# Performance work log

Hardware: AMD Instinct MI355X
Metric: run time of the kernel (lower is better)

Reference implementation:

```python
import jax, jax.numpy as jnp
import numpy as np

B, S, H, D = 2, 2048, 16, 64

def setup_inputs() -> dict:
    key = jax.random.key(0)
    kq, kk, kv = jax.random.split(key, 3)
    query = jax.random.normal(kq, (B, S, H, D), dtype=jnp.float32)
    k_ = jax.random.normal(kk, (B, S, H, D), dtype=jnp.float32)
    v_ = jax.random.normal(kv, (B, S, H, D), dtype=jnp.float32)
    return {"query": query, "key": k_, "value": v_}

def reference(query, key, value):
    # AsyncLongContextAttention with world_size=1 degenerates to full
    # softmax attention over the global sequence (all2all / ring are
    # pure data movement). Defaults: causal=False, dropout_p=0.0,
    # softmax_scale = 1/sqrt(head_dim) (flash-attn convention).
    scale = 1.0 / jnp.sqrt(jnp.asarray(query.shape[-1], query.dtype))
    # scores: [B, H, Sq, Sk]
    scores = jnp.einsum("bqhd,bkhd->bhqk", query, key) * scale
    probs = jax.nn.softmax(scores, axis=-1)
    # out: [B, Sq, H, D]
    out = jnp.einsum("bhqk,bkhd->bqhd", probs, value)
    return out
```

## Files before the change

kernel.cpp:

```cpp
#include <hip/hip_runtime.h>
#include <math.h>

using half8  = __attribute__((ext_vector_type(8))) _Float16;
using half4  = __attribute__((ext_vector_type(4))) _Float16;
using fp16x2 = __attribute__((ext_vector_type(2))) __fp16;
using f32x4  = __attribute__((ext_vector_type(4))) float;

namespace {
constexpr int NB = 2, NS = 2048, NH = 16, ND = 64;
constexpr int QBLK = 128, KVBLK = 64;
constexpr int RS = NH * ND;
constexpr int NT = NS / KVBLK;
constexpr size_t TILEH = 4096;
constexpr size_t TILEB = TILEH * 2;
constexpr size_t SCR_HALFS = (size_t)NB * NH * NT * TILEH;

__device__ __forceinline__ int sidx(int row, int col) {
    return row * 64 + (col ^ (((row & 7) ^ ((row >> 3) & 7)) << 3));
}
__device__ __forceinline__ int kperm(int k) {
    return 16 * (2 * (k >> 5) + ((k >> 2) & 1)) + 4 * ((k >> 3) & 3) + (k & 3);
}
__device__ __forceinline__ float ex2(float x) {
#if __has_builtin(__builtin_amdgcn_exp2f)
    return __builtin_amdgcn_exp2f(x);
#else
    return exp2f(x);
#endif
}
__device__ __forceinline__ half8 pk8(const float4& a, const float4& b) {
    half8 r;
    fp16x2* h = (fp16x2*)&r;
    h[0] = __builtin_amdgcn_cvt_pkrtz(a.x, a.y);
    h[1] = __builtin_amdgcn_cvt_pkrtz(a.z, a.w);
    h[2] = __builtin_amdgcn_cvt_pkrtz(b.x, b.y);
    h[3] = __builtin_amdgcn_cvt_pkrtz(b.z, b.w);
    return r;
}
__device__ __forceinline__ half8 pk8s(const float4& a, const float4& b, float s) {
    half8 r;
    fp16x2* h = (fp16x2*)&r;
    h[0] = __builtin_amdgcn_cvt_pkrtz(a.x * s, a.y * s);
    h[1] = __builtin_amdgcn_cvt_pkrtz(a.z * s, a.w * s);
    h[2] = __builtin_amdgcn_cvt_pkrtz(b.x * s, b.y * s);
    h[3] = __builtin_amdgcn_cvt_pkrtz(b.z * s, b.w * s);
    return r;
}
__device__ __forceinline__ half8 pk8v(const float* v) {
    half8 r;
    fp16x2* h = (fp16x2*)&r;
    h[0] = __builtin_amdgcn_cvt_pkrtz(v[0], v[1]);
    h[1] = __builtin_amdgcn_cvt_pkrtz(v[2], v[3]);
    h[2] = __builtin_amdgcn_cvt_pkrtz(v[4], v[5]);
    h[3] = __builtin_amdgcn_cvt_pkrtz(v[6], v[7]);
    return r;
}
__device__ __forceinline__ half8 pkq(const f32x4& a, const f32x4& b) {
    half8 r;
    fp16x2* h = (fp16x2*)&r;
    h[0] = __builtin_amdgcn_cvt_pkrtz(a[0], a[1]);
    h[1] = __builtin_amdgcn_cvt_pkrtz(a[2], a[3]);
    h[2] = __builtin_amdgcn_cvt_pkrtz(b[0], b[1]);
    h[3] = __builtin_amdgcn_cvt_pkrtz(b[2], b[3]);
    return r;
}
__device__ __forceinline__ void gld16(const void* g, void* l) {
    __builtin_amdgcn_global_load_lds(
        (const __attribute__((address_space(1))) void*)g,
        (__attribute__((address_space(3))) void*)l, 16, 0, 0);
}
}

__global__ __launch_bounds__(512)
void prep_kernel(const float* __restrict__ Kg, const float* __restrict__ Vg,
                 _Float16* __restrict__ Kscr, _Float16* __restrict__ Vscr) {
    const int t  = threadIdx.x;
    const int bh = blockIdx.x;
    const int kt = blockIdx.y;
    const int b  = bh >> 4;
    const int h  = bh & 15;
    const size_t tile = ((size_t)bh * NT + kt) * TILEH;

    {
        const int row = t >> 3;
        const int sc0 = (t & 7) * 8;
        const int m   = kperm(row);
        const int kg  = m >> 4, mlc = m & 15;
        const int ks  = sc0 >> 5, mlg = (sc0 >> 3) & 3;
        const float* kp = Kg + (size_t)(b * NS + kt * KVBLK + row) * RS + h * ND + sc0;
        *(half8*)&Kscr[tile + (size_t)((ks * 4 + kg) * 64 + mlg * 16 + mlc) * 8] =
            pk8(*(const float4*)kp, *(const float4*)(kp + 4));
    }
    {
        const int c   = t >> 6;
        const int vl  = t & 63;
        const int vlc = vl & 15, vlg = vl >> 4;
        const int ks  = c >> 2, dg = c & 3;
        const float* vp = Vg + (size_t)(b * NS + kt * KVBLK + 32 * ks + 8 * vlg) * RS
                             + h * ND + 16 * dg + vlc;
        float vv[8];
#pragma unroll
        for (int j = 0; j < 8; ++j) vv[j] = vp[(size_t)j * RS];
        *(half8*)&Vscr[tile + (size_t)(c * 64 + vl) * 8] = pk8v(vv);
    }
}

__global__ __launch_bounds__(512, 4)
void fattn_kernel(const float* __restrict__ Qg, const _Float16* __restrict__ Kscr,
                  const _Float16* __restrict__ Vscr, float* __restrict__ Og) {
    __shared__ __align__(16) _Float16 KT[4][KVBLK * ND];
    __shared__ __align__(16) _Float16 VT[4][KVBLK * ND];
    __shared__ float SL[4 * 2 * 64];

    const int t  = threadIdx.x;
    const int l  = t & 63;
    const int w  = t >> 6;
    const int lc = l & 15;
    const int lg = l >> 4;
    const int parity = w >> 2;
    const int wq = (w & 3) * 32;
    const int bh = blockIdx.x;
    const int qt = blockIdx.y;
    const int b  = bh >> 4;
    const int h  = bh & 15;
    const int lofs = l * 8;

    const float SC = 0.18033688011112042f;
    half8 qfr[2][2];
#pragma unroll
    for (int f = 0; f < 2; ++f) {
        const int qrow = qt * QBLK + wq + f * 16 + lc;
        const float* qp = Qg + (size_t)(b * NS + qrow) * RS + h * ND;
#pragma unroll
        for (int ks = 0; ks < 2; ++ks) {
            const float* p = qp + 32 * ks + 8 * lg;
            qfr[f][ks] = pk8s(*(const float4*)p, *(const float4*)(p + 4), SC);
        }
    }

    const f32x4 ZERO = {0.f, 0.f, 0.f, 0.f};
    f32x4 acc[4][2];
    float lsum[2] = {0.f, 0.f};
#pragma unroll
    for (int dg = 0; dg < 4; ++dg) { acc[dg][0] = ZERO; acc[dg][1] = ZERO; }

    const char* ksrc = (const char*)(Kscr + (size_t)bh * NT * TILEH) + t * 16;
    const char* vsrc = (const char*)(Vscr + (size_t)bh * NT * TILEH) + t * 16;

    auto STEP = [&](const _Float16* KTb, const _Float16* VTb,
                    _Float16* kA, _Float16* kB, _Float16* vA, _Float16* vB,
                    const char* gkA, const char* gkB,
                    const char* gvA, const char* gvB, bool issue) {
        if (issue) {
            gld16(gkA, kA + w * 512);
            gld16(gkB, kB + w * 512);
            gld16(gvA, vA + w * 512);
            gld16(gvB, vB + w * 512);
        }
        f32x4 st[4][2];
        __builtin_amdgcn_s_setprio(1);
#pragma unroll
        for (int kg = 0; kg < 4; ++kg) {
            const half8 kf = *(const half8*)&KTb[kg * 512 + lofs];
            st[kg][0] = __builtin_amdgcn_mfma_f32_16x16x32_f16(kf, qfr[0][0], ZERO, 0, 0, 0);
            st[kg][1] = __builtin_amdgcn_mfma_f32_16x16x32_f16(kf, qfr[1][0], ZERO, 0, 0, 0);
        }
#pragma unroll
        for (int kg = 0; kg < 4; ++kg) {
            const half8 kf = *(const half8*)&KTb[(4 + kg) * 512 + lofs];
            st[kg][0] = __builtin_amdgcn_mfma_f32_16x16x32_f16(kf, qfr[0][1], st[kg][0], 0, 0, 0);
            st[kg][1] = __builtin_amdgcn_mfma_f32_16x16x32_f16(kf, qfr[1][1], st[kg][1], 0, 0, 0);
        }
        __builtin_amdgcn_s_setprio(0);

#pragma unroll
        for (int kg = 0; kg < 4; ++kg)
#pragma unroll
            for (int f = 0; f < 2; ++f)
#pragma unroll
                for (int r = 0; r < 4; ++r) {
                    st[kg][f][r] = ex2(st[kg][f][r]);
                    lsum[f] += st[kg][f][r];
                }
        const half8 pA0 = pkq(st[0][0], st[1][0]);
        const half8 pA1 = pkq(st[0][1], st[1][1]);
        const half8 pB0 = pkq(st[2][0], st[3][0]);
        const half8 pB1 = pkq(st[2][1], st[3][1]);

        __builtin_amdgcn_s_setprio(1);
#pragma unroll
        for (int dg = 0; dg < 4; ++dg) {
            const half8 vf0 = *(const half8*)&VTb[dg * 512 + lofs];
            acc[dg][0] = __builtin_amdgcn_mfma_f32_16x16x32_f16(vf0, pA0, acc[dg][0], 0, 0, 0);
            acc[dg][1] = __builtin_amdgcn_mfma_f32_16x16x32_f16(vf0, pA1, acc[dg][1], 0, 0, 0);
        }
#pragma unroll
        for (int dg = 0; dg < 4; ++dg) {
            const half8 vf1 = *(const half8*)&VTb[(4 + dg) * 512 + lofs];
            acc[dg][0] = __builtin_amdgcn_mfma_f32_16x16x32_f16(vf1, pB0, acc[dg][0], 0, 0, 0);
            acc[dg][1] = __builtin_amdgcn_mfma_f32_16x16x32_f16(vf1, pB1, acc[dg][1], 0, 0, 0);
        }
        __builtin_amdgcn_s_setprio(0);
        __syncthreads();
    };

    gld16(ksrc, &KT[0][w * 512]);
    gld16(ksrc + TILEB, &KT[1][w * 512]);
    gld16(vsrc, &VT[0][w * 512]);
    gld16(vsrc + TILEB, &VT[1][w * 512]);
    __syncthreads();

    const char* kcur = ksrc + 2 * TILEB;
    const char* vcur = vsrc + 2 * TILEB;
    for (int s = 0; s < 16; s += 2) {
        STEP(&KT[parity][0], &VT[parity][0],
             &KT[2][0], &KT[3][0], &VT[2][0], &VT[3][0],
             kcur, kcur + TILEB, vcur, vcur + TILEB, true);
        STEP(&KT[2 + parity][0], &VT[2 + parity][0],
             &KT[0][0], &KT[1][0], &VT[0][0], &VT[1][0],
             kcur + 2 * TILEB, kcur + 3 * TILEB,
             vcur + 2 * TILEB, vcur + 3 * TILEB, s + 2 < 16);
        kcur += 4 * TILEB;
        vcur += 4 * TILEB;
    }

#pragma unroll
    for (int f = 0; f < 2; ++f) {
        lsum[f] += __shfl_xor(lsum[f], 16);
        lsum[f] += __shfl_xor(lsum[f], 32);
    }

    float* sf = (float*)&KT[0][0];
    if (parity) {
        const int uw = w - 4;
#pragma unroll
        for (int dg = 0; dg < 4; ++dg)
#pragma unroll
            for (int f = 0; f < 2; ++f)
                *(float4*)&sf[((uw * 8 + dg * 2 + f) * 64 + l) * 4] = *(float4*)&acc[dg][f];
        SL[(uw * 2 + 0) * 64 + l] = lsum[0];
        SL[(uw * 2 + 1) * 64 + l] = lsum[1];
    }
    __syncthreads();
    if (!parity) {
#pragma unroll
        for (int dg = 0; dg < 4; ++dg)
#pragma unroll
            for (int f = 0; f < 2; ++f) {
                const float4 o = *(const float4*)&sf[((w * 8 + dg * 2 + f) * 64 + l) * 4];
                acc[dg][f][0] += o.x; acc[dg][f][1] += o.y;
                acc[dg][f][2] += o.z; acc[dg][f][3] += o.w;
            }
        const float ls[2] = {lsum[0] + SL[(w * 2 + 0) * 64 + l],
                             lsum[1] + SL[(w * 2 + 1) * 64 + l]};
#pragma unroll
        for (int f = 0; f < 2; ++f) {
            const float inv  = 1.0f / ls[f];
            const int   qrow = qt * QBLK + wq + f * 16 + lc;
            float* op = Og + (size_t)(b * NS + qrow) * RS + h * ND;
#pragma unroll
            for (int dg = 0; dg < 4; ++dg) {
                float4 o;
                o.x = acc[dg][f][0] * inv;
                o.y = acc[dg][f][1] * inv;
                o.z = acc[dg][f][2] * inv;
                o.w = acc[dg][f][3] * inv;
                *(float4*)(op + 16 * dg + 4 * lg) = o;
            }
        }
    }
}

__global__ __launch_bounds__(512, 4)
void fattn_fb(const float* __restrict__ Qg, const float* __restrict__ Kg,
              const float* __restrict__ Vg, float* __restrict__ Og) {
    __shared__ __align__(16) _Float16 KT[2][KVBLK * ND];
    __shared__ __align__(16) _Float16 VT[2][KVBLK * ND];
    __shared__ __align__(16) _Float16 PS[8][16 * ND];
    const int t = threadIdx.x, l = t & 63, w = t >> 6, lc = l & 15, lg = l >> 4;
    const int bh = blockIdx.x, qt = blockIdx.y, b = bh >> 4, h = bh & 15;
    const float SC = 0.18033688011112042f;
    const int qrow = qt * QBLK + w * 16 + lc;
    half8 qfr[2];
    {
        const float* qp = Qg + (size_t)(b * NS + qrow) * RS + h * ND;
#pragma unroll
        for (int ks = 0; ks < 2; ++ks) {
            const float* p = qp + 32 * ks + 8 * lg;
            qfr[ks] = pk8s(*(const float4*)p, *(const float4*)(p + 4), SC);
        }
    }
    float mrun = -INFINITY, lrun = 0.f;
    const f32x4 zero4 = {0.f, 0.f, 0.f, 0.f};
    f32x4 acc[4];
#pragma unroll
    for (int dg = 0; dg < 4; ++dg) acc[dg] = zero4;
    const int srow = t >> 3, sc0 = (t & 7) * 8;
    const float* kbase = Kg + (size_t)(b * NS) * RS + h * ND + sc0;
    const float* vbase = Vg + (size_t)(b * NS + 8 * w) * RS + h * ND + l;
    float4 kr[2]; float vv[8];
    auto LOAD = [&](int kt) {
        const float* kp = kbase + (size_t)(kt * KVBLK + srow) * RS;
        kr[0] = *(const float4*)(kp + 0);
        kr[1] = *(const float4*)(kp + 4);
        const float* vp = vbase + (size_t)(kt * KVBLK) * RS;
#pragma unroll
        for (int i = 0; i < 8; ++i) vv[i] = vp[(size_t)i * RS];
    };
    auto STORE = [&](int p) {
        *(half8*)&KT[p][sidx(srow, sc0)] = pk8(kr[0], kr[1]);
        *(half8*)&VT[p][sidx(l, 8 * w)]  = pk8v(vv);
    };
    LOAD(0); STORE(0);
    __syncthreads();
    for (int kt = 0; kt < NT; ++kt) {
        const int p = kt & 1;
        if (kt + 1 < NT) LOAD(kt + 1);
        f32x4 st[4];
#pragma unroll
        for (int kg = 0; kg < 4; ++kg) st[kg] = zero4;
#pragma unroll
        for (int ks = 0; ks < 2; ++ks)
#pragma unroll
            for (int kg = 0; kg < 4; ++kg) {
                const half8 kf = *(const half8*)&KT[p][sidx(16 * kg + lc, 32 * ks + 8 * lg)];
                st[kg] = __builtin_amdgcn_mfma_f32_16x16x32_f16(kf, qfr[ks], st[kg], 0, 0, 0);
            }
        {
            float tm = -INFINITY;
#pragma unroll
            for (int kg = 0; kg < 4; ++kg)
#pragma unroll
                for (int r = 0; r < 4; ++r) tm = fmaxf(tm, st[kg][r]);
            tm = fmaxf(tm, __shfl_xor(tm, 16));
            tm = fmaxf(tm, __shfl_xor(tm, 32));
            if (!__all(tm <= mrun)) {
                const float mn = fmaxf(mrun, tm);
                const float corr = exp2f(mrun - mn);
                mrun = mn; lrun *= corr;
#pragma unroll
                for (int dg = 0; dg < 4; ++dg)
#pragma unroll
                    for (int r = 0; r < 4; ++r) acc[dg][r] *= corr;
            }
            float rs = 0.f;
#pragma unroll
            for (int kg = 0; kg < 4; ++kg)
#pragma unroll
                for (int r = 0; r < 4; ++r) {
                    const float pv = exp2f(st[kg][r] - mrun);
                    st[kg][r] = pv; rs += pv;
                }
            rs += __shfl_xor(rs, 16);
            rs += __shfl_xor(rs, 32);
            lrun += rs;
#pragma unroll
            for (int kg = 0; kg < 4; ++kg) {
                half4 ph; fp16x2* hp = (fp16x2*)&ph;
                hp[0] = __builtin_amdgcn_cvt_pkrtz(st[kg][0], st[kg][1]);
                hp[1] = __builtin_amdgcn_cvt_pkrtz(st[kg][2], st[kg][3]);
                *(half4*)&PS[w][sidx(lc, 16 * kg + 4 * lg)] = ph;
            }
        }
#pragma unroll
        for (int ks = 0; ks < 2; ++ks) {
            const half8 pf = *(const half8*)&PS[w][sidx(lc, 32 * ks + 8 * lg)];
#pragma unroll
            for (int dg = 0; dg < 4; ++dg) {
                const half8 vf = *(const half8*)&VT[p][sidx(16 * dg + lc, 32 * ks + 8 * lg)];
                acc[dg] = __builtin_amdgcn_mfma_f32_16x16x32_f16(vf, pf, acc[dg], 0, 0, 0);
            }
        }
        if (kt + 1 < NT) STORE(p ^ 1);
        __syncthreads();
    }
    {
        const float inv = 1.0f / lrun;
        float* op = Og + (size_t)(b * NS + qrow) * RS + h * ND;
#pragma unroll
        for (int dg = 0; dg < 4; ++dg) {
            float4 o;
            o.x = acc[dg][0] * inv; o.y = acc[dg][1] * inv;
            o.z = acc[dg][2] * inv; o.w = acc[dg][3] * inv;
            *(float4*)(op + 16 * dg + 4 * lg) = o;
        }
    }
}

extern "C" void kernel_launch(void* const* d_in, const int* in_sizes, int n_in,
                              void* d_out, int out_size, void* d_ws, size_t ws_size,
                              hipStream_t stream) {
    const float* Q = (const float*)d_in[0];
    const float* K = (const float*)d_in[1];
    const float* V = (const float*)d_in[2];
    float* O = (float*)d_out;
    const size_t need = 2 * SCR_HALFS * sizeof(_Float16);
    if (ws_size >= need) {
        _Float16* Kscr = (_Float16*)d_ws;
        _Float16* Vscr = Kscr + SCR_HALFS;
        prep_kernel<<<dim3(NB * NH, NT), dim3(512), 0, stream>>>(K, V, Kscr, Vscr);
        fattn_kernel<<<dim3(NB * NH, NS / QBLK), dim3(512), 0, stream>>>(Q, Kscr, Vscr, O);
    } else {
        fattn_fb<<<dim3(NB * NH, NS / QBLK), dim3(512), 0, stream>>>(Q, K, V, O);
    }
}
```

Before: 53.07 us.

## Split KV across four wave classes with 1024-thread blocks and 32-row tiles

The attention kernel now uses 1024 threads per block: four wave classes per 32-row query group, each taking a different 32-key tile out of a 128-key step. The old version used two parity halves over 64-key tiles. The prep kernel repacks K and V into 32-row tiles to match. The partial accumulators and row sums are combined through shared memory in a two-stage tree reduction. This raises the number of waves working on each query tile to hide latency. In exchange, each wave does less MFMA work per barrier and the reduction needs extra barriers.

```diff
diff --git a/kernel.cpp b/kernel.cpp
--- a/kernel.cpp
+++ b/kernel.cpp
@@ -8,18 +8,19 @@
 
 namespace {
 constexpr int NB = 2, NS = 2048, NH = 16, ND = 64;
-constexpr int QBLK = 128, KVBLK = 64;
+constexpr int QBLK = 128;
+constexpr int KVB = 32;
+constexpr int NTIL = NS / KVB;
 constexpr int RS = NH * ND;
-constexpr int NT = NS / KVBLK;
-constexpr size_t TILEH = 4096;
-constexpr size_t TILEB = TILEH * 2;
-constexpr size_t SCR_HALFS = (size_t)NB * NH * NT * TILEH;
+constexpr size_t TIL_H = 2048;
+constexpr size_t STEPB = 16384;
+constexpr size_t SCR_HALFS = (size_t)NB * NH * NTIL * TIL_H;
 
 __device__ __forceinline__ int sidx(int row, int col) {
     return row * 64 + (col ^ (((row & 7) ^ ((row >> 3) & 7)) << 3));
 }
-__device__ __forceinline__ int kperm(int k) {
-    return 16 * (2 * (k >> 5) + ((k >> 2) & 1)) + 4 * ((k >> 3) & 3) + (k & 3);
+__device__ __forceinline__ int kperm32(int k) {
+    return 16 * ((k >> 2) & 1) + 4 * ((k >> 3) & 3) + (k & 3);
 }
 __device__ __forceinline__ float ex2(float x) {
 #if __has_builtin(__builtin_amdgcn_exp2f)
@@ -71,7 +72,7 @@
 }
 }
 
-__global__ __launch_bounds__(512)
+__global__ __launch_bounds__(256)
 void prep_kernel(const float* __restrict__ Kg, const float* __restrict__ Vg,
                  _Float16* __restrict__ Kscr, _Float16* __restrict__ Vscr) {
     const int t  = threadIdx.x;
@@ -79,25 +80,24 @@
     const int kt = blockIdx.y;
     const int b  = bh >> 4;
     const int h  = bh & 15;
-    const size_t tile = ((size_t)bh * NT + kt) * TILEH;
+    const size_t tile = ((size_t)bh * NTIL + kt) * TIL_H;
 
     {
         const int row = t >> 3;
         const int sc0 = (t & 7) * 8;
-        const int m   = kperm(row);
+        const int m   = kperm32(row);
         const int kg  = m >> 4, mlc = m & 15;
         const int ks  = sc0 >> 5, mlg = (sc0 >> 3) & 3;
-        const float* kp = Kg + (size_t)(b * NS + kt * KVBLK + row) * RS + h * ND + sc0;
-        *(half8*)&Kscr[tile + (size_t)((ks * 4 + kg) * 64 + mlg * 16 + mlc) * 8] =
+        const float* kp = Kg + (size_t)(b * NS + kt * KVB + row) * RS + h * ND + sc0;
+        *(half8*)&Kscr[tile + (size_t)((ks * 2 + kg) * 64 + mlg * 16 + mlc) * 8] =
             pk8(*(const float4*)kp, *(const float4*)(kp + 4));
     }
     {
         const int c   = t >> 6;
         const int vl  = t & 63;
         const int vlc = vl & 15, vlg = vl >> 4;
-        const int ks  = c >> 2, dg = c & 3;
-        const float* vp = Vg + (size_t)(b * NS + kt * KVBLK + 32 * ks + 8 * vlg) * RS
-                             + h * ND + 16 * dg + vlc;
+        const float* vp = Vg + (size_t)(b * NS + kt * KVB + 8 * vlg) * RS
+                             + h * ND + 16 * c + vlc;
         float vv[8];
 #pragma unroll
         for (int j = 0; j < 8; ++j) vv[j] = vp[(size_t)j * RS];
@@ -105,20 +105,21 @@
     }
 }
 
-__global__ __launch_bounds__(512, 4)
+__global__ __launch_bounds__(1024, 4)
 void fattn_kernel(const float* __restrict__ Qg, const _Float16* __restrict__ Kscr,
                   const _Float16* __restrict__ Vscr, float* __restrict__ Og) {
-    __shared__ __align__(16) _Float16 KT[4][KVBLK * ND];
-    __shared__ __align__(16) _Float16 VT[4][KVBLK * ND];
-    __shared__ float SL[4 * 2 * 64];
+    __shared__ __align__(16) _Float16 KT[2][8192];
+    __shared__ __align__(16) _Float16 VT[2][8192];
+    __shared__ float SL[1024];
 
     const int t  = threadIdx.x;
     const int l  = t & 63;
     const int w  = t >> 6;
     const int lc = l & 15;
     const int lg = l >> 4;
-    const int parity = w >> 2;
-    const int wq = (w & 3) * 32;
+    const int cls = w & 3;
+    const int qg  = w >> 2;
+    const int wq  = qg * 32;
     const int bh = blockIdx.x;
     const int qt = blockIdx.y;
     const int b  = bh >> 4;
@@ -144,37 +145,33 @@
 #pragma unroll
     for (int dg = 0; dg < 4; ++dg) { acc[dg][0] = ZERO; acc[dg][1] = ZERO; }
 
-    const char* ksrc = (const char*)(Kscr + (size_t)bh * NT * TILEH) + t * 16;
-    const char* vsrc = (const char*)(Vscr + (size_t)bh * NT * TILEH) + t * 16;
+    const char* ksrc = (const char*)(Kscr + (size_t)bh * NTIL * TIL_H) + t * 16;
+    const char* vsrc = (const char*)(Vscr + (size_t)bh * NTIL * TIL_H) + t * 16;
 
     auto STEP = [&](const _Float16* KTb, const _Float16* VTb,
-                    _Float16* kA, _Float16* kB, _Float16* vA, _Float16* vB,
-                    const char* gkA, const char* gkB,
-                    const char* gvA, const char* gvB, bool issue) {
+                    _Float16* kD, _Float16* vD, size_t srcOff, bool issue) {
         if (issue) {
-            gld16(gkA, kA + w * 512);
-            gld16(gkB, kB + w * 512);
-            gld16(gvA, vA + w * 512);
-            gld16(gvB, vB + w * 512);
-        }
-        f32x4 st[4][2];
+            gld16(ksrc + srcOff, kD + w * 512);
+            gld16(vsrc + srcOff, vD + w * 512);
+        }
+        f32x4 st[2][2];
         __builtin_amdgcn_s_setprio(1);
 #pragma unroll
-        for (int kg = 0; kg < 4; ++kg) {
+        for (int kg = 0; kg < 2; ++kg) {
             const half8 kf = *(const half8*)&KTb[kg * 512 + lofs];
             st[kg][0] = __builtin_amdgcn_mfma_f32_16x16x32_f16(kf, qfr[0][0], ZERO, 0, 0, 0);
             st[kg][1] = __builtin_amdgcn_mfma_f32_16x16x32_f16(kf, qfr[1][0], ZERO, 0, 0, 0);
         }
 #pragma unroll
-        for (int kg = 0; kg < 4; ++kg) {
-            const half8 kf = *(const half8*)&KTb[(4 + kg) * 512 + lofs];
+        for (int kg = 0; kg < 2; ++kg) {
+            const half8 kf = *(const half8*)&KTb[(2 + kg) * 512 + lofs];
             st[kg][0] = __builtin_amdgcn_mfma_f32_16x16x32_f16(kf, qfr[0][1], st[kg][0], 0, 0, 0);
             st[kg][1] = __builtin_amdgcn_mfma_f32_16x16x32_f16(kf, qfr[1][1], st[kg][1], 0, 0, 0);
         }
         __builtin_amdgcn_s_setprio(0);
 
 #pragma unroll
-        for (int kg = 0; kg < 4; ++kg)
+        for (int kg = 0; kg < 2; ++kg)
 #pragma unroll
             for (int f = 0; f < 2; ++f)
 #pragma unroll
@@ -182,80 +179,103 @@
                     st[kg][f][r] = ex2(st[kg][f][r]);
                     lsum[f] += st[kg][f][r];
                 }
-        const half8 pA0 = pkq(st[0][0], st[1][0]);
-        const half8 pA1 = pkq(st[0][1], st[1][1]);
-        const half8 pB0 = pkq(st[2][0], st[3][0]);
-        const half8 pB1 = pkq(st[2][1], st[3][1]);
+        const half8 pf0 = pkq(st[0][0], st[1][0]);
+        const half8 pf1 = pkq(st[0][1], st[1][1]);
 
         __builtin_amdgcn_s_setprio(1);
 #pragma unroll
         for (int dg = 0; dg < 4; ++dg) {
-            const half8 vf0 = *(const half8*)&VTb[dg * 512 + lofs];
-            acc[dg][0] = __builtin_amdgcn_mfma_f32_16x16x32_f16(vf0, pA0, acc[dg][0], 0, 0, 0);
-            acc[dg][1] = __builtin_amdgcn_mfma_f32_16x16x32_f16(vf0, pA1, acc[dg][1], 0, 0, 0);
-        }
-#pragma unroll
-        for (int dg = 0; dg < 4; ++dg) {
-            const half8 vf1 = *(const half8*)&VTb[(4 + dg) * 512 + lofs];
-            acc[dg][0] = __builtin_amdgcn_mfma_f32_16x16x32_f16(vf1, pB0, acc[dg][0], 0, 0, 0);
-            acc[dg][1] = __builtin_amdgcn_mfma_f32_16x16x32_f16(vf1, pB1, acc[dg][1], 0, 0, 0);
+            const half8 vf = *(const half8*)&VTb[dg * 512 + lofs];
+            acc[dg][0] = __builtin_amdgcn_mfma_f32_16x16x32_f16(vf, pf0, acc[dg][0], 0, 0, 0);
+            acc[dg][1] = __builtin_amdgcn_mfma_f32_16x16x32_f16(vf, pf1, acc[dg][1], 0, 0, 0);
         }
         __builtin_amdgcn_s_setprio(0);
         __syncthreads();
     };
 
     gld16(ksrc, &KT[0][w * 512]);
-    gld16(ksrc + TILEB, &KT[1][w * 512]);
     gld16(vsrc, &VT[0][w * 512]);
-    gld16(vsrc + TILEB, &VT[1][w * 512]);
     __syncthreads();
 
-    const char* kcur = ksrc + 2 * TILEB;
-    const char* vcur = vsrc + 2 * TILEB;
     for (int s = 0; s < 16; s += 2) {
-        STEP(&KT[parity][0], &VT[parity][0],
-             &KT[2][0], &KT[3][0], &VT[2][0], &VT[3][0],
-             kcur, kcur + TILEB, vcur, vcur + TILEB, true);
-        STEP(&KT[2 + parity][0], &VT[2 + parity][0],
-             &KT[0][0], &KT[1][0], &VT[0][0], &VT[1][0],
-             kcur + 2 * TILEB, kcur + 3 * TILEB,
-             vcur + 2 * TILEB, vcur + 3 * TILEB, s + 2 < 16);
-        kcur += 4 * TILEB;
-        vcur += 4 * TILEB;
-    }
-
-#pragma unroll
-    for (int f = 0; f < 2; ++f) {
-        lsum[f] += __shfl_xor(lsum[f], 16);
-        lsum[f] += __shfl_xor(lsum[f], 32);
-    }
-
-    float* sf = (float*)&KT[0][0];
-    if (parity) {
-        const int uw = w - 4;
+        STEP(&KT[0][cls * 2048], &VT[0][cls * 2048],
+             &KT[1][0], &VT[1][0], (size_t)(s + 1) * STEPB, true);
+        STEP(&KT[1][cls * 2048], &VT[1][cls * 2048],
+             &KT[0][0], &VT[0][0], (size_t)(s + 2) * STEPB, s + 2 < 16);
+    }
+
+    float* sfA = (float*)&KT[0][0];
+    float* sfB = (float*)&VT[0][0];
+    if (cls == 2) {
 #pragma unroll
         for (int dg = 0; dg < 4; ++dg)
 #pragma unroll
             for (int f = 0; f < 2; ++f)
-                *(float4*)&sf[((uw * 8 + dg * 2 + f) * 64 + l) * 4] = *(float4*)&acc[dg][f];
-        SL[(uw * 2 + 0) * 64 + l] = lsum[0];
-        SL[(uw * 2 + 1) * 64 + l] = lsum[1];
+                *(float4*)&sfA[((qg * 8 + dg * 2 + f) * 64 + l) * 4] = *(float4*)&acc[dg][f];
+        SL[(qg * 2 + 0) * 64 + l] = lsum[0];
+        SL[(qg * 2 + 1) * 64 + l] = lsum[1];
+    }
+    if (cls == 3) {
+#pragma unroll
+        for (int dg = 0; dg < 4; ++dg)
+#pragma unroll
+            for (int f = 0; f < 2; ++f)
+                *(float4*)&sfB[((qg * 8 + dg * 2 + f) * 64 + l) * 4] = *(float4*)&acc[dg][f];
+        SL[512 + (qg * 2 + 0) * 64 + l] = lsum[0];
+        SL[512 + (qg * 2 + 1) * 64 + l] = lsum[1];
     }
     __syncthreads();
-    if (!parity) {
+    if (cls == 0) {
 #pragma unroll
         for (int dg = 0; dg < 4; ++dg)
 #pragma unroll
             for (int f = 0; f < 2; ++f) {
-                const float4 o = *(const float4*)&sf[((w * 8 + dg * 2 + f) * 64 + l) * 4];
+                const float4 o = *(const float4*)&sfA[((qg * 8 + dg * 2 + f) * 64 + l) * 4];
                 acc[dg][f][0] += o.x; acc[dg][f][1] += o.y;
                 acc[dg][f][2] += o.z; acc[dg][f][3] += o.w;
             }
-        const float ls[2] = {lsum[0] + SL[(w * 2 + 0) * 64 + l],
-                             lsum[1] + SL[(w * 2 + 1) * 64 + l]};
+        lsum[0] += SL[(qg * 2 + 0) * 64 + l];
+        lsum[1] += SL[(qg * 2 + 1) * 64 + l];
+    }
+    if (cls == 1) {
+#pragma unroll
+        for (int dg = 0; dg < 4; ++dg)
+#pragma unroll
+            for (int f = 0; f < 2; ++f) {
+                const float4 o = *(const float4*)&sfB[((qg * 8 + dg * 2 + f) * 64 + l) * 4];
+                acc[dg][f][0] += o.x; acc[dg][f][1] += o.y;
+                acc[dg][f][2] += o.z; acc[dg][f][3] += o.w;
+            }
+        lsum[0] += SL[512 + (qg * 2 + 0) * 64 + l];
+        lsum[1] += SL[512 + (qg * 2 + 1) * 64 + l];
+    }
+    __syncthreads();
+    if (cls == 1) {
+#pragma unroll
+        for (int dg = 0; dg < 4; ++dg)
+#pragma unroll
+            for (int f = 0; f < 2; ++f)
+                *(float4*)&sfA[((qg * 8 + dg * 2 + f) * 64 + l) * 4] = *(float4*)&acc[dg][f];
+        SL[(qg * 2 + 0) * 64 + l] = lsum[0];
+        SL[(qg * 2 + 1) * 64 + l] = lsum[1];
+    }
+    __syncthreads();
+    if (cls == 0) {
+#pragma unroll
+        for (int dg = 0; dg < 4; ++dg)
+#pragma unroll
+            for (int f = 0; f < 2; ++f) {
+                const float4 o = *(const float4*)&sfA[((qg * 8 + dg * 2 + f) * 64 + l) * 4];
+                acc[dg][f][0] += o.x; acc[dg][f][1] += o.y;
+                acc[dg][f][2] += o.z; acc[dg][f][3] += o.w;
+            }
+        lsum[0] += SL[(qg * 2 + 0) * 64 + l];
+        lsum[1] += SL[(qg * 2 + 1) * 64 + l];
 #pragma unroll
         for (int f = 0; f < 2; ++f) {
-            const float inv  = 1.0f / ls[f];
+            lsum[f] += __shfl_xor(lsum[f], 16);
+            lsum[f] += __shfl_xor(lsum[f], 32);
+            const float inv  = 1.0f / lsum[f];
             const int   qrow = qt * QBLK + wq + f * 16 + lc;
             float* op = Og + (size_t)(b * NS + qrow) * RS + h * ND;
 #pragma unroll
@@ -274,6 +294,8 @@
 __global__ __launch_bounds__(512, 4)
 void fattn_fb(const float* __restrict__ Qg, const float* __restrict__ Kg,
               const float* __restrict__ Vg, float* __restrict__ Og) {
+    constexpr int KVBLK = 64;
+    constexpr int NT = NS / KVBLK;
     __shared__ __align__(16) _Float16 KT[2][KVBLK * ND];
     __shared__ __align__(16) _Float16 VT[2][KVBLK * ND];
     __shared__ __align__(16) _Float16 PS[8][16 * ND];
@@ -398,8 +420,8 @@
     if (ws_size >= need) {
         _Float16* Kscr = (_Float16*)d_ws;
         _Float16* Vscr = Kscr + SCR_HALFS;
-        prep_kernel<<<dim3(NB * NH, NT), dim3(512), 0, stream>>>(K, V, Kscr, Vscr);
-        fattn_kernel<<<dim3(NB * NH, NS / QBLK), dim3(512), 0, stream>>>(Q, Kscr, Vscr, O);
+        prep_kernel<<<dim3(NB * NH, NTIL), dim3(256), 0, stream>>>(K, V, Kscr, Vscr);
+        fattn_kernel<<<dim3(NB * NH, NS / QBLK), dim3(1024), 0, stream>>>(Q, Kscr, Vscr, O);
     } else {
         fattn_fb<<<dim3(NB * NH, NS / QBLK), dim3(512), 0, stream>>>(Q, K, V, O);
     }
```

Measured after the change: 57.76 us. +8.8%, slower.

## Double query rows per wave to reuse K/V fragments across four MFMA tiles

Applied to the files above, without the earlier changes.

Each wave now processes 64 query rows (four 16-row fragments) instead of 32, doubling the query block to 256 rows per workgroup. Each K/V fragment loaded from LDS feeds twice as many MFMAs, and total K/V tile traffic per output halves. The cost is higher register pressure (launch bounds lowered to 2 blocks/CU), half as many workgroups, and a larger cross-wave reduction that now spills into both K and V shared buffers. The fallback kernel keeps its original 128-row block size.

```diff
diff --git a/kernel.cpp b/kernel.cpp
--- a/kernel.cpp
+++ b/kernel.cpp
@@ -8,7 +8,7 @@
 
 namespace {
 constexpr int NB = 2, NS = 2048, NH = 16, ND = 64;
-constexpr int QBLK = 128, KVBLK = 64;
+constexpr int QBLK = 256, KVBLK = 64;
 constexpr int RS = NH * ND;
 constexpr int NT = NS / KVBLK;
 constexpr size_t TILEH = 4096;
@@ -105,12 +105,12 @@
     }
 }
 
-__global__ __launch_bounds__(512, 4)
+__global__ __launch_bounds__(512, 2)
 void fattn_kernel(const float* __restrict__ Qg, const _Float16* __restrict__ Kscr,
                   const _Float16* __restrict__ Vscr, float* __restrict__ Og) {
     __shared__ __align__(16) _Float16 KT[4][KVBLK * ND];
     __shared__ __align__(16) _Float16 VT[4][KVBLK * ND];
-    __shared__ float SL[4 * 2 * 64];
+    __shared__ float SL[4 * 4 * 64];
 
     const int t  = threadIdx.x;
     const int l  = t & 63;
@@ -118,7 +118,7 @@
     const int lc = l & 15;
     const int lg = l >> 4;
     const int parity = w >> 2;
-    const int wq = (w & 3) * 32;
+    const int wq = (w & 3) * 64;
     const int bh = blockIdx.x;
     const int qt = blockIdx.y;
     const int b  = bh >> 4;
@@ -126,9 +126,9 @@
     const int lofs = l * 8;
 
     const float SC = 0.18033688011112042f;
-    half8 qfr[2][2];
-#pragma unroll
-    for (int f = 0; f < 2; ++f) {
+    half8 qfr[4][2];
+#pragma unroll
+    for (int f = 0; f < 4; ++f) {
         const int qrow = qt * QBLK + wq + f * 16 + lc;
         const float* qp = Qg + (size_t)(b * NS + qrow) * RS + h * ND;
 #pragma unroll
@@ -139,10 +139,12 @@
     }
 
     const f32x4 ZERO = {0.f, 0.f, 0.f, 0.f};
-    f32x4 acc[4][2];
-    float lsum[2] = {0.f, 0.f};
-#pragma unroll
-    for (int dg = 0; dg < 4; ++dg) { acc[dg][0] = ZERO; acc[dg][1] = ZERO; }
+    f32x4 acc[4][4];
+    float lsum[4] = {0.f, 0.f, 0.f, 0.f};
+#pragma unroll
+    for (int dg = 0; dg < 4; ++dg)
+#pragma unroll
+        for (int f = 0; f < 4; ++f) acc[dg][f] = ZERO;
 
     const char* ksrc = (const char*)(Kscr + (size_t)bh * NT * TILEH) + t * 16;
     const char* vsrc = (const char*)(Vscr + (size_t)bh * NT * TILEH) + t * 16;
@@ -157,48 +159,54 @@
             gld16(gvA, vA + w * 512);
             gld16(gvB, vB + w * 512);
         }
-        f32x4 st[4][2];
+        f32x4 st[4][4];
         __builtin_amdgcn_s_setprio(1);
 #pragma unroll
         for (int kg = 0; kg < 4; ++kg) {
             const half8 kf = *(const half8*)&KTb[kg * 512 + lofs];
-            st[kg][0] = __builtin_amdgcn_mfma_f32_16x16x32_f16(kf, qfr[0][0], ZERO, 0, 0, 0);
-            st[kg][1] = __builtin_amdgcn_mfma_f32_16x16x32_f16(kf, qfr[1][0], ZERO, 0, 0, 0);
+#pragma unroll
+            for (int f = 0; f < 4; ++f)
+                st[kg][f] = __builtin_amdgcn_mfma_f32_16x16x32_f16(kf, qfr[f][0], ZERO, 0, 0, 0);
         }
 #pragma unroll
         for (int kg = 0; kg < 4; ++kg) {
             const half8 kf = *(const half8*)&KTb[(4 + kg) * 512 + lofs];
-            st[kg][0] = __builtin_amdgcn_mfma_f32_16x16x32_f16(kf, qfr[0][1], st[kg][0], 0, 0, 0);
-            st[kg][1] = __builtin_amdgcn_mfma_f32_16x16x32_f16(kf, qfr[1][1], st[kg][1], 0, 0, 0);
+#pragma unroll
+            for (int f = 0; f < 4; ++f)
+                st[kg][f] = __builtin_amdgcn_mfma_f32_16x16x32_f16(kf, qfr[f][1], st[kg][f], 0, 0, 0);
         }
         __builtin_amdgcn_s_setprio(0);
 
 #pragma unroll
         for (int kg = 0; kg < 4; ++kg)
 #pragma unroll
-            for (int f = 0; f < 2; ++f)
+            for (int f = 0; f < 4; ++f)
 #pragma unroll
                 for (int r = 0; r < 4; ++r) {
                     st[kg][f][r] = ex2(st[kg][f][r]);
                     lsum[f] += st[kg][f][r];
                 }
-        const half8 pA0 = pkq(st[0][0], st[1][0]);
-        const half8 pA1 = pkq(st[0][1], st[1][1]);
-        const half8 pB0 = pkq(st[2][0], st[3][0]);
-        const half8 pB1 = pkq(st[2][1], st[3][1]);
+        half8 pA[4], pB[4];
+#pragma unroll
+        for (int f = 0; f < 4; ++f) {
+            pA[f] = pkq(st[0][f], st[1][f]);
+            pB[f] = pkq(st[2][f], st[3][f]);
+        }
 
         __builtin_amdgcn_s_setprio(1);
 #pragma unroll
         for (int dg = 0; dg < 4; ++dg) {
             const half8 vf0 = *(const half8*)&VTb[dg * 512 + lofs];
-            acc[dg][0] = __builtin_amdgcn_mfma_f32_16x16x32_f16(vf0, pA0, acc[dg][0], 0, 0, 0);
-            acc[dg][1] = __builtin_amdgcn_mfma_f32_16x16x32_f16(vf0, pA1, acc[dg][1], 0, 0, 0);
+#pragma unroll
+            for (int f = 0; f < 4; ++f)
+                acc[dg][f] = __builtin_amdgcn_mfma_f32_16x16x32_f16(vf0, pA[f], acc[dg][f], 0, 0, 0);
         }
 #pragma unroll
         for (int dg = 0; dg < 4; ++dg) {
             const half8 vf1 = *(const half8*)&VTb[(4 + dg) * 512 + lofs];
-            acc[dg][0] = __builtin_amdgcn_mfma_f32_16x16x32_f16(vf1, pB0, acc[dg][0], 0, 0, 0);
-            acc[dg][1] = __builtin_amdgcn_mfma_f32_16x16x32_f16(vf1, pB1, acc[dg][1], 0, 0, 0);
+#pragma unroll
+            for (int f = 0; f < 4; ++f)
+                acc[dg][f] = __builtin_amdgcn_mfma_f32_16x16x32_f16(vf1, pB[f], acc[dg][f], 0, 0, 0);
         }
         __builtin_amdgcn_s_setprio(0);
         __syncthreads();
@@ -225,37 +233,42 @@
     }
 
 #pragma unroll
-    for (int f = 0; f < 2; ++f) {
+    for (int f = 0; f < 4; ++f) {
         lsum[f] += __shfl_xor(lsum[f], 16);
         lsum[f] += __shfl_xor(lsum[f], 32);
     }
 
-    float* sf = (float*)&KT[0][0];
+    float* sfA = (float*)&KT[0][0];
+    float* sfB = (float*)&VT[0][0];
     if (parity) {
         const int uw = w - 4;
 #pragma unroll
         for (int dg = 0; dg < 4; ++dg)
 #pragma unroll
-            for (int f = 0; f < 2; ++f)
-                *(float4*)&sf[((uw * 8 + dg * 2 + f) * 64 + l) * 4] = *(float4*)&acc[dg][f];
-        SL[(uw * 2 + 0) * 64 + l] = lsum[0];
-        SL[(uw * 2 + 1) * 64 + l] = lsum[1];
+            for (int f = 0; f < 4; ++f) {
+                float* dst = (dg < 2) ? sfA : sfB;
+                *(float4*)&dst[(((uw * 2 + (dg & 1)) * 4 + f) * 64 + l) * 4] =
+                    *(float4*)&acc[dg][f];
+            }
+#pragma unroll
+        for (int f = 0; f < 4; ++f) SL[(uw * 4 + f) * 64 + l] = lsum[f];
     }
     __syncthreads();
     if (!parity) {
 #pragma unroll
         for (int dg = 0; dg < 4; ++dg)
 #pragma unroll
-            for (int f = 0; f < 2; ++f) {
-                const float4 o = *(const float4*)&sf[((w * 8 + dg * 2 + f) * 64 + l) * 4];
+            for (int f = 0; f < 4; ++f) {
+                const float* src = (dg < 2) ? sfA : sfB;
+                const float4 o =
+                    *(const float4*)&src[(((w * 2 + (dg & 1)) * 4 + f) * 64 + l) * 4];
                 acc[dg][f][0] += o.x; acc[dg][f][1] += o.y;
                 acc[dg][f][2] += o.z; acc[dg][f][3] += o.w;
             }
-        const float ls[2] = {lsum[0] + SL[(w * 2 + 0) * 64 + l],
-                             lsum[1] + SL[(w * 2 + 1) * 64 + l]};
-#pragma unroll
-        for (int f = 0; f < 2; ++f) {
-            const float inv  = 1.0f / ls[f];
+#pragma unroll
+        for (int f = 0; f < 4; ++f) {
+            const float ls = lsum[f] + SL[(w * 4 + f) * 64 + l];
+            const float inv  = 1.0f / ls;
             const int   qrow = qt * QBLK + wq + f * 16 + lc;
             float* op = Og + (size_t)(b * NS + qrow) * RS + h * ND;
 #pragma unroll
@@ -274,13 +287,14 @@
 __global__ __launch_bounds__(512, 4)
 void fattn_fb(const float* __restrict__ Qg, const float* __restrict__ Kg,
               const float* __restrict__ Vg, float* __restrict__ Og) {
+    constexpr int FQB = 128;
     __shared__ __align__(16) _Float16 KT[2][KVBLK * ND];
     __shared__ __align__(16) _Float16 VT[2][KVBLK * ND];
     __shared__ __align__(16) _Float16 PS[8][16 * ND];
     const int t = threadIdx.x, l = t & 63, w = t >> 6, lc = l & 15, lg = l >> 4;
     const int bh = blockIdx.x, qt = blockIdx.y, b = bh >> 4, h = bh & 15;
     const float SC = 0.18033688011112042f;
-    const int qrow = qt * QBLK + w * 16 + lc;
+    const int qrow = qt * FQB + w * 16 + lc;
     half8 qfr[2];
     {
         const float* qp = Qg + (size_t)(b * NS + qrow) * RS + h * ND;
@@ -401,6 +415,6 @@
         prep_kernel<<<dim3(NB * NH, NT), dim3(512), 0, stream>>>(K, V, Kscr, Vscr);
         fattn_kernel<<<dim3(NB * NH, NS / QBLK), dim3(512), 0, stream>>>(Q, Kscr, Vscr, O);
     } else {
-        fattn_fb<<<dim3(NB * NH, NS / QBLK), dim3(512), 0, stream>>>(Q, K, V, O);
-    }
-}
+        fattn_fb<<<dim3(NB * NH, NS / 128), dim3(512), 0, stream>>>(Q, K, V, O);
+    }
+}
```

Result: no change. 53.74 us (+1.3%).
